# Optimization experiments

Measured on AMD Instinct MI355X. Metric: run time of the kernel, lower is better.

## Reference

```python
import jax, jax.numpy as jnp
import numpy as np

N_NODES = 50000
N_EDGES = 800000
D_FEAT = 64


def setup_inputs() -> dict:
    key = jax.random.key(0)
    k1, k2, k3 = jax.random.split(key, 3)
    xs = jax.random.normal(k1, (N_NODES, D_FEAT), dtype=jnp.float32)
    src = jax.random.randint(k2, (N_EDGES,), 0, N_NODES, dtype=jnp.int32)
    dst = jax.random.randint(k3, (N_EDGES,), 0, N_NODES, dtype=jnp.int32)
    return {"xs": xs, "src": src, "dst": dst}


def reference(xs, src, dst):
    # Edge-list scatter-mean: for each edge (src=ee, dst=i), accumulate
    # xs[ee] into bucket i, then divide by the bucket count.
    gathered = xs[src]                                   # [E, D]
    sums = jax.ops.segment_sum(gathered, dst, num_segments=N_NODES)  # [N, D]
    counts = jax.ops.segment_sum(
        jnp.ones((src.shape[0],), dtype=xs.dtype), dst, num_segments=N_NODES
    )                                                    # [N]
    # Original only emits groups that appear; here empty groups yield 0.
    return sums / jnp.maximum(counts, 1.0)[:, None]
```

## Files before the change

### kernel.cpp

```cpp
#include <hip/hip_runtime.h>

#define N_NODES 50000
#define N_EDGES 800000
#define D_FEAT 64

#define NPART 200
#define EPP (N_EDGES / NPART)
#define BIG_SHIFT 9
#define BIG_NODES 512
#define NBIG ((N_NODES + BIG_NODES - 1) / BIG_NODES)
#define SCAP 12288

__global__ __launch_bounds__(1024) void part_hist_kernel(const int* __restrict__ dst,
                                                         int* __restrict__ histBB) {
    __shared__ int h[NBIG];
    int t = threadIdx.x, blk = blockIdx.x;
    if (t < NBIG) h[t] = 0;
    __syncthreads();
    int base = blk * EPP;
    for (int i = t; i < EPP; i += 1024)
        atomicAdd(&h[dst[base + i] >> BIG_SHIFT], 1);
    __syncthreads();
    if (t < NBIG) histBB[blk * NBIG + t] = h[t];
}

__global__ void col_scan_kernel(const int* __restrict__ histBB,
                                int* __restrict__ baseBB,
                                int* __restrict__ binTot) {
    __shared__ int lds[256];
    int bin = blockIdx.x, t = threadIdx.x;
    int v = (t < NPART) ? histBB[t * NBIG + bin] : 0;
    lds[t] = v;
    __syncthreads();
    for (int off = 1; off < 256; off <<= 1) {
        int x = (t >= off) ? lds[t - off] : 0;
        __syncthreads();
        lds[t] += x;
        __syncthreads();
    }
    if (t < NPART) baseBB[t * NBIG + bin] = lds[t] - v;
    if (t == 255) binTot[bin] = lds[255];
}

__global__ void bin_scan_kernel(const int* __restrict__ binTot, int* __restrict__ binBase) {
    __shared__ int wsum[2];
    int t = threadIdx.x;
    int v = (t < NBIG) ? binTot[t] : 0;
    int lane = t & 63, wave = t >> 6;
    int incl = v;
    #pragma unroll
    for (int o = 1; o < 64; o <<= 1) { int x = __shfl_up(incl, o); if (lane >= o) incl += x; }
    if (lane == 63) wsum[wave] = incl;
    __syncthreads();
    int base = (wave == 1) ? wsum[0] : 0;
    if (t < NBIG) binBase[t] = base + incl - v;
    if (t == NBIG - 1) binBase[NBIG] = base + incl;
}

__global__ __launch_bounds__(1024) void part_scatter_kernel(const int* __restrict__ src,
                                                            const int* __restrict__ dst,
                                                            const int* __restrict__ baseBB,
                                                            const int* __restrict__ binBase,
                                                            unsigned int* __restrict__ staging) {
    __shared__ int cur[NBIG];
    int t = threadIdx.x, blk = blockIdx.x;
    if (t < NBIG) cur[t] = binBase[t] + baseBB[blk * NBIG + t];
    __syncthreads();
    int base = blk * EPP;
    for (int i = t; i < EPP; i += 1024) {
        int d = dst[base + i];
        int bin = d >> BIG_SHIFT;
        int pos = atomicAdd(&cur[bin], 1);
        staging[pos] = (unsigned int)src[base + i] |
                       ((unsigned int)(d & (BIG_NODES - 1)) << 16);
    }
}

__global__ __launch_bounds__(512) void sort512_kernel(const unsigned int* __restrict__ staging,
                                                      const int* __restrict__ binBase,
                                                      unsigned short* __restrict__ esorted,
                                                      int* __restrict__ offs) {
    __shared__ int cnt[BIG_NODES];
    __shared__ int cur[BIG_NODES];
    __shared__ unsigned short list[SCAP];
    __shared__ int wsum[8];
    int bin = blockIdx.x, t = threadIdx.x;
    int lo = binBase[bin], hi = binBase[bin + 1];
    int n = hi - lo;
    int nodeLo = bin << BIG_SHIFT;

    cnt[t] = 0;
    __syncthreads();
    for (int i = lo + t; i < hi; i += 512)
        atomicAdd(&cnt[(staging[i] >> 16) & (BIG_NODES - 1)], 1);
    __syncthreads();

    int v = cnt[t];
    int lane = t & 63, wave = t >> 6;
    int incl = v;
    #pragma unroll
    for (int o = 1; o < 64; o <<= 1) { int x = __shfl_up(incl, o); if (lane >= o) incl += x; }
    if (lane == 63) wsum[wave] = incl;
    __syncthreads();
    int wbase = 0;
    #pragma unroll
    for (int w = 0; w < 8; ++w) wbase += (w < wave) ? wsum[w] : 0;
    int excl = wbase + incl - v;
    cur[t] = excl;

    int node = nodeLo + t;
    if (node < N_NODES) offs[node] = lo + excl;
    if (bin == NBIG - 1 && t == 0) offs[N_NODES] = N_EDGES;
    __syncthreads();

    if (n <= SCAP) {
        for (int i = lo + t; i < hi; i += 512) {
            unsigned int pk = staging[i];
            int p = atomicAdd(&cur[(pk >> 16) & (BIG_NODES - 1)], 1);
            list[p] = (unsigned short)pk;
        }
        __syncthreads();
        for (int i = t; i < n; i += 512)
            esorted[lo + i] = list[i];
    } else {
        for (int i = lo + t; i < hi; i += 512) {
            unsigned int pk = staging[i];
            int p = atomicAdd(&cur[(pk >> 16) & (BIG_NODES - 1)], 1);
            esorted[lo + p] = (unsigned short)pk;
        }
    }
}

__global__ __launch_bounds__(256) void csr_pull_kernel(const float* __restrict__ xs,
                                                       const unsigned short* __restrict__ esorted,
                                                       const int* __restrict__ offs,
                                                       float* __restrict__ out) {
    int tid = blockIdx.x * 256 + threadIdx.x;
    int node = tid >> 4;
    int c = tid & 15;
    int beg = offs[node];
    int end = offs[node + 1];
    int deg = end - beg;
    float4 acc = make_float4(0.f, 0.f, 0.f, 0.f);
    for (int j0 = 0; j0 < deg; j0 += 16) {
        int rem = deg - j0;
        int m = rem < 16 ? rem : 16;
        int myid = (c < m) ? (int)__builtin_nontemporal_load(esorted + beg + j0 + c) : 0;
        if (m == 16) {
            #pragma unroll
            for (int k = 0; k < 16; ++k) {
                int s = __shfl(myid, k, 16);
                const float4 v = *reinterpret_cast<const float4*>(xs + s * D_FEAT + c * 4);
                acc.x += v.x; acc.y += v.y; acc.z += v.z; acc.w += v.w;
            }
        } else {
            for (int k = 0; k < m; ++k) {
                int s = __shfl(myid, k, 16);
                const float4 v = *reinterpret_cast<const float4*>(xs + s * D_FEAT + c * 4);
                acc.x += v.x; acc.y += v.y; acc.z += v.z; acc.w += v.w;
            }
        }
    }
    float inv = 1.0f / fmaxf((float)deg, 1.0f);
    float* op = out + (size_t)node * D_FEAT + c * 4;
    __builtin_nontemporal_store(acc.x * inv, op + 0);
    __builtin_nontemporal_store(acc.y * inv, op + 1);
    __builtin_nontemporal_store(acc.z * inv, op + 2);
    __builtin_nontemporal_store(acc.w * inv, op + 3);
}


__global__ void scatter_kernel(const float* __restrict__ xs,
                               const int* __restrict__ src,
                               const int* __restrict__ dst,
                               float* __restrict__ sums,
                               float* __restrict__ counts) {
    int tid = blockIdx.x * blockDim.x + threadIdx.x;
    int e = tid >> 4;
    int c = tid & 15;
    if (e >= N_EDGES) return;
    int s = src[e];
    int d = dst[e];
    const float4 v = *reinterpret_cast<const float4*>(xs + (size_t)s * D_FEAT + c * 4);
    float* outp = sums + (size_t)d * D_FEAT + c * 4;
    atomicAdd(outp + 0, v.x);
    atomicAdd(outp + 1, v.y);
    atomicAdd(outp + 2, v.z);
    atomicAdd(outp + 3, v.w);
    if (c == 0) atomicAdd(counts + d, 1.0f);
}

__global__ void divide_kernel(float* __restrict__ out, const float* __restrict__ counts) {
    int tid = blockIdx.x * blockDim.x + threadIdx.x;
    if (tid >= N_NODES * D_FEAT / 4) return;
    int node = tid >> 4;
    float inv = 1.0f / fmaxf(counts[node], 1.0f);
    float4 v = reinterpret_cast<const float4*>(out)[tid];
    v.x *= inv; v.y *= inv; v.z *= inv; v.w *= inv;
    reinterpret_cast<float4*>(out)[tid] = v;
}


extern "C" void kernel_launch(void* const* d_in, const int* in_sizes, int n_in,
                              void* d_out, int out_size, void* d_ws, size_t ws_size,
                              hipStream_t stream) {
    const float* xs  = (const float*)d_in[0];
    const int*   src = (const int*)d_in[1];
    const int*   dst = (const int*)d_in[2];
    float* out = (float*)d_out;

    size_t need = (size_t)(2 * NPART * NBIG + NBIG + (NBIG + 1) + (N_NODES + 1)) * sizeof(int)
                + (size_t)N_EDGES * sizeof(unsigned int)
                + (size_t)N_EDGES * sizeof(unsigned short);
    if (ws_size < need) {
        float* counts = (float*)d_ws;
        hipMemsetAsync(out, 0, (size_t)N_NODES * D_FEAT * sizeof(float), stream);
        hipMemsetAsync(counts, 0, (size_t)N_NODES * sizeof(float), stream);
        scatter_kernel<<<(N_EDGES * 16 + 255) / 256, 256, 0, stream>>>(xs, src, dst, out, counts);
        divide_kernel<<<(N_NODES * D_FEAT / 4 + 255) / 256, 256, 0, stream>>>(out, counts);
        return;
    }

    int* ws = (int*)d_ws;
    int* histBB  = ws;
    int* baseBB  = histBB + NPART * NBIG;
    int* binTot  = baseBB + NPART * NBIG;
    int* binBase = binTot + NBIG;
    int* offs    = binBase + NBIG + 1;
    unsigned int* staging = (unsigned int*)(offs + N_NODES + 1);
    unsigned short* esorted = (unsigned short*)(staging + N_EDGES);

    part_hist_kernel<<<NPART, 1024, 0, stream>>>(dst, histBB);
    col_scan_kernel<<<NBIG, 256, 0, stream>>>(histBB, baseBB, binTot);
    bin_scan_kernel<<<1, 128, 0, stream>>>(binTot, binBase);
    part_scatter_kernel<<<NPART, 1024, 0, stream>>>(src, dst, baseBB, binBase, staging);
    sort512_kernel<<<NBIG, 512, 0, stream>>>(staging, binBase, esorted, offs);
    csr_pull_kernel<<<(N_NODES * 16) / 256, 256, 0, stream>>>(xs, esorted, offs, out);
}
```

Before: 124.4 us.

## Fuse CSR build phases into one cooperative kernel with grid syncs

```diff
diff --git a/kernel.cpp b/kernel.cpp
--- a/kernel.cpp
+++ b/kernel.cpp
@@ -1,4 +1,7 @@
 #include <hip/hip_runtime.h>
+#include <hip/hip_cooperative_groups.h>
+
+namespace cg = cooperative_groups;
 
 #define N_NODES 50000
 #define N_EDGES 800000
@@ -9,125 +12,114 @@
 #define BIG_SHIFT 9
 #define BIG_NODES 512
 #define NBIG ((N_NODES + BIG_NODES - 1) / BIG_NODES)
-#define SCAP 12288
-
-__global__ __launch_bounds__(1024) void part_hist_kernel(const int* __restrict__ dst,
-                                                         int* __restrict__ histBB) {
-    __shared__ int h[NBIG];
-    int t = threadIdx.x, blk = blockIdx.x;
-    if (t < NBIG) h[t] = 0;
-    __syncthreads();
-    int base = blk * EPP;
-    for (int i = t; i < EPP; i += 1024)
-        atomicAdd(&h[dst[base + i] >> BIG_SHIFT], 1);
-    __syncthreads();
-    if (t < NBIG) histBB[blk * NBIG + t] = h[t];
-}
-
-__global__ void col_scan_kernel(const int* __restrict__ histBB,
-                                int* __restrict__ baseBB,
-                                int* __restrict__ binTot) {
-    __shared__ int lds[256];
-    int bin = blockIdx.x, t = threadIdx.x;
-    int v = (t < NPART) ? histBB[t * NBIG + bin] : 0;
-    lds[t] = v;
-    __syncthreads();
-    for (int off = 1; off < 256; off <<= 1) {
-        int x = (t >= off) ? lds[t - off] : 0;
-        __syncthreads();
-        lds[t] += x;
-        __syncthreads();
-    }
-    if (t < NPART) baseBB[t * NBIG + bin] = lds[t] - v;
-    if (t == 255) binTot[bin] = lds[255];
-}
-
-__global__ void bin_scan_kernel(const int* __restrict__ binTot, int* __restrict__ binBase) {
-    __shared__ int wsum[2];
+#define GRID_BUILD 200
+
+__global__ __launch_bounds__(256, 4) void build_kernel(
+    const int* __restrict__ src, const int* __restrict__ dst,
+    int* __restrict__ histBB, int* __restrict__ baseBB,
+    int* __restrict__ binTot, int* __restrict__ binBase,
+    int* __restrict__ offs,
+    unsigned int* __restrict__ staging,
+    unsigned short* __restrict__ esorted)
+{
+    cg::grid_group grid = cg::this_grid();
+    __shared__ int sa[512];
+    __shared__ int sb[512];
     int t = threadIdx.x;
-    int v = (t < NBIG) ? binTot[t] : 0;
-    int lane = t & 63, wave = t >> 6;
-    int incl = v;
-    #pragma unroll
-    for (int o = 1; o < 64; o <<= 1) { int x = __shfl_up(incl, o); if (lane >= o) incl += x; }
-    if (lane == 63) wsum[wave] = incl;
-    __syncthreads();
-    int base = (wave == 1) ? wsum[0] : 0;
-    if (t < NBIG) binBase[t] = base + incl - v;
-    if (t == NBIG - 1) binBase[NBIG] = base + incl;
-}
-
-__global__ __launch_bounds__(1024) void part_scatter_kernel(const int* __restrict__ src,
-                                                            const int* __restrict__ dst,
-                                                            const int* __restrict__ baseBB,
-                                                            const int* __restrict__ binBase,
-                                                            unsigned int* __restrict__ staging) {
-    __shared__ int cur[NBIG];
-    int t = threadIdx.x, blk = blockIdx.x;
-    if (t < NBIG) cur[t] = binBase[t] + baseBB[blk * NBIG + t];
-    __syncthreads();
-    int base = blk * EPP;
-    for (int i = t; i < EPP; i += 1024) {
-        int d = dst[base + i];
-        int bin = d >> BIG_SHIFT;
-        int pos = atomicAdd(&cur[bin], 1);
-        staging[pos] = (unsigned int)src[base + i] |
-                       ((unsigned int)(d & (BIG_NODES - 1)) << 16);
-    }
-}
-
-__global__ __launch_bounds__(512) void sort512_kernel(const unsigned int* __restrict__ staging,
-                                                      const int* __restrict__ binBase,
-                                                      unsigned short* __restrict__ esorted,
-                                                      int* __restrict__ offs) {
-    __shared__ int cnt[BIG_NODES];
-    __shared__ int cur[BIG_NODES];
-    __shared__ unsigned short list[SCAP];
-    __shared__ int wsum[8];
-    int bin = blockIdx.x, t = threadIdx.x;
-    int lo = binBase[bin], hi = binBase[bin + 1];
-    int n = hi - lo;
-    int nodeLo = bin << BIG_SHIFT;
-
-    cnt[t] = 0;
-    __syncthreads();
-    for (int i = lo + t; i < hi; i += 512)
-        atomicAdd(&cnt[(staging[i] >> 16) & (BIG_NODES - 1)], 1);
-    __syncthreads();
-
-    int v = cnt[t];
-    int lane = t & 63, wave = t >> 6;
-    int incl = v;
-    #pragma unroll
-    for (int o = 1; o < 64; o <<= 1) { int x = __shfl_up(incl, o); if (lane >= o) incl += x; }
-    if (lane == 63) wsum[wave] = incl;
-    __syncthreads();
-    int wbase = 0;
-    #pragma unroll
-    for (int w = 0; w < 8; ++w) wbase += (w < wave) ? wsum[w] : 0;
-    int excl = wbase + incl - v;
-    cur[t] = excl;
-
-    int node = nodeLo + t;
-    if (node < N_NODES) offs[node] = lo + excl;
-    if (bin == NBIG - 1 && t == 0) offs[N_NODES] = N_EDGES;
-    __syncthreads();
-
-    if (n <= SCAP) {
-        for (int i = lo + t; i < hi; i += 512) {
+
+    for (int p = blockIdx.x; p < NPART; p += gridDim.x) {
+        if (t < NBIG) sa[t] = 0;
+        __syncthreads();
+        int base = p * EPP;
+        for (int i = t; i < EPP; i += 256)
+            atomicAdd(&sa[dst[base + i] >> BIG_SHIFT], 1);
+        __syncthreads();
+        if (t < NBIG) histBB[p * NBIG + t] = sa[t];
+        __syncthreads();
+    }
+    grid.sync();
+
+    for (int bin = blockIdx.x; bin < NBIG; bin += gridDim.x) {
+        int v = (t < NPART) ? histBB[t * NBIG + bin] : 0;
+        sa[t] = v;
+        __syncthreads();
+        for (int off = 1; off < 256; off <<= 1) {
+            int x = (t >= off) ? sa[t - off] : 0;
+            __syncthreads();
+            sa[t] += x;
+            __syncthreads();
+        }
+        if (t < NPART) baseBB[t * NBIG + bin] = sa[t] - v;
+        if (t == 255) binTot[bin] = sa[255];
+        __syncthreads();
+    }
+    grid.sync();
+
+    if (blockIdx.x == 0) {
+        int v = (t < NBIG) ? binTot[t] : 0;
+        int lane = t & 63, wave = t >> 6;
+        int incl = v;
+        #pragma unroll
+        for (int o = 1; o < 64; o <<= 1) { int x = __shfl_up(incl, o); if (lane >= o) incl += x; }
+        if (lane == 63) sb[wave] = incl;
+        __syncthreads();
+        int wbase = 0;
+        #pragma unroll
+        for (int w = 0; w < 4; ++w) wbase += (w < wave) ? sb[w] : 0;
+        if (t < NBIG) binBase[t] = wbase + incl - v;
+        if (t == NBIG - 1) binBase[NBIG] = wbase + incl;
+    }
+    grid.sync();
+
+    for (int p = blockIdx.x; p < NPART; p += gridDim.x) {
+        if (t < NBIG) sa[t] = binBase[t] + baseBB[p * NBIG + t];
+        __syncthreads();
+        int base = p * EPP;
+        for (int i = t; i < EPP; i += 256) {
+            int d = dst[base + i];
+            int bin = d >> BIG_SHIFT;
+            int pos = atomicAdd(&sa[bin], 1);
+            staging[pos] = (unsigned int)src[base + i] |
+                           ((unsigned int)(d & (BIG_NODES - 1)) << 16);
+        }
+        __syncthreads();
+    }
+    grid.sync();
+
+    for (int bin = blockIdx.x; bin < NBIG; bin += gridDim.x) {
+        int lo = binBase[bin], hi = binBase[bin + 1];
+        sa[t] = 0; sa[t + 256] = 0;
+        __syncthreads();
+        for (int i = lo + t; i < hi; i += 256)
+            atomicAdd(&sa[(staging[i] >> 16) & (BIG_NODES - 1)], 1);
+        __syncthreads();
+        int c0 = sa[2 * t], c1 = sa[2 * t + 1];
+        int pv = c0 + c1;
+        int lane = t & 63, wave = t >> 6;
+        int incl = pv;
+        #pragma unroll
+        for (int o = 1; o < 64; o <<= 1) { int x = __shfl_up(incl, o); if (lane >= o) incl += x; }
+        if (lane == 63) sb[wave] = incl;
+        __syncthreads();
+        int wbase = 0;
+        #pragma unroll
+        for (int w = 0; w < 4; ++w) wbase += (w < wave) ? sb[w] : 0;
+        int eh = wbase + incl - pv;
+        __syncthreads();
+        int e0 = eh, e1 = eh + c0;
+        sb[2 * t] = lo + e0;
+        sb[2 * t + 1] = lo + e1;
+        int node = (bin << BIG_SHIFT) + 2 * t;
+        if (node < N_NODES) offs[node] = lo + e0;
+        if (node + 1 < N_NODES) offs[node + 1] = lo + e1;
+        if (bin == NBIG - 1 && t == 0) offs[N_NODES] = N_EDGES;
+        __syncthreads();
+        for (int i = lo + t; i < hi; i += 256) {
             unsigned int pk = staging[i];
-            int p = atomicAdd(&cur[(pk >> 16) & (BIG_NODES - 1)], 1);
-            list[p] = (unsigned short)pk;
+            int p = atomicAdd(&sb[(pk >> 16) & (BIG_NODES - 1)], 1);
+            esorted[p] = (unsigned short)pk;
         }
         __syncthreads();
-        for (int i = t; i < n; i += 512)
-            esorted[lo + i] = list[i];
-    } else {
-        for (int i = lo + t; i < hi; i += 512) {
-            unsigned int pk = staging[i];
-            int p = atomicAdd(&cur[(pk >> 16) & (BIG_NODES - 1)], 1);
-            esorted[lo + p] = (unsigned short)pk;
-        }
     }
 }
 
@@ -170,34 +162,108 @@
 }
 
 
-__global__ void scatter_kernel(const float* __restrict__ xs,
-                               const int* __restrict__ src,
-                               const int* __restrict__ dst,
-                               float* __restrict__ sums,
-                               float* __restrict__ counts) {
-    int tid = blockIdx.x * blockDim.x + threadIdx.x;
-    int e = tid >> 4;
-    int c = tid & 15;
-    if (e >= N_EDGES) return;
-    int s = src[e];
-    int d = dst[e];
-    const float4 v = *reinterpret_cast<const float4*>(xs + (size_t)s * D_FEAT + c * 4);
-    float* outp = sums + (size_t)d * D_FEAT + c * 4;
-    atomicAdd(outp + 0, v.x);
-    atomicAdd(outp + 1, v.y);
-    atomicAdd(outp + 2, v.z);
-    atomicAdd(outp + 3, v.w);
-    if (c == 0) atomicAdd(counts + d, 1.0f);
-}
-
-__global__ void divide_kernel(float* __restrict__ out, const float* __restrict__ counts) {
-    int tid = blockIdx.x * blockDim.x + threadIdx.x;
-    if (tid >= N_NODES * D_FEAT / 4) return;
-    int node = tid >> 4;
-    float inv = 1.0f / fmaxf(counts[node], 1.0f);
-    float4 v = reinterpret_cast<const float4*>(out)[tid];
-    v.x *= inv; v.y *= inv; v.z *= inv; v.w *= inv;
-    reinterpret_cast<float4*>(out)[tid] = v;
+__global__ __launch_bounds__(1024) void part_hist_kernel(const int* __restrict__ dst,
+                                                         int* __restrict__ histBB) {
+    __shared__ int h[NBIG];
+    int t = threadIdx.x, blk = blockIdx.x;
+    if (t < NBIG) h[t] = 0;
+    __syncthreads();
+    int base = blk * EPP;
+    for (int i = t; i < EPP; i += 1024)
+        atomicAdd(&h[dst[base + i] >> BIG_SHIFT], 1);
+    __syncthreads();
+    if (t < NBIG) histBB[blk * NBIG + t] = h[t];
+}
+
+__global__ void col_scan_kernel(const int* __restrict__ histBB,
+                                int* __restrict__ baseBB,
+                                int* __restrict__ binTot) {
+    __shared__ int lds[256];
+    int bin = blockIdx.x, t = threadIdx.x;
+    int v = (t < NPART) ? histBB[t * NBIG + bin] : 0;
+    lds[t] = v;
+    __syncthreads();
+    for (int off = 1; off < 256; off <<= 1) {
+        int x = (t >= off) ? lds[t - off] : 0;
+        __syncthreads();
+        lds[t] += x;
+        __syncthreads();
+    }
+    if (t < NPART) baseBB[t * NBIG + bin] = lds[t] - v;
+    if (t == 255) binTot[bin] = lds[255];
+}
+
+__global__ void bin_scan_kernel(const int* __restrict__ binTot, int* __restrict__ binBase) {
+    __shared__ int wsum[2];
+    int t = threadIdx.x;
+    int v = (t < NBIG) ? binTot[t] : 0;
+    int lane = t & 63, wave = t >> 6;
+    int incl = v;
+    #pragma unroll
+    for (int o = 1; o < 64; o <<= 1) { int x = __shfl_up(incl, o); if (lane >= o) incl += x; }
+    if (lane == 63) wsum[wave] = incl;
+    __syncthreads();
+    int base = (wave == 1) ? wsum[0] : 0;
+    if (t < NBIG) binBase[t] = base + incl - v;
+    if (t == NBIG - 1) binBase[NBIG] = base + incl;
+}
+
+__global__ __launch_bounds__(1024) void part_scatter_kernel(const int* __restrict__ src,
+                                                            const int* __restrict__ dst,
+                                                            const int* __restrict__ baseBB,
+                                                            const int* __restrict__ binBase,
+                                                            unsigned int* __restrict__ staging) {
+    __shared__ int cur[NBIG];
+    int t = threadIdx.x, blk = blockIdx.x;
+    if (t < NBIG) cur[t] = binBase[t] + baseBB[blk * NBIG + t];
+    __syncthreads();
+    int base = blk * EPP;
+    for (int i = t; i < EPP; i += 1024) {
+        int d = dst[base + i];
+        int bin = d >> BIG_SHIFT;
+        int pos = atomicAdd(&cur[bin], 1);
+        staging[pos] = (unsigned int)src[base + i] |
+                       ((unsigned int)(d & (BIG_NODES - 1)) << 16);
+    }
+}
+
+__global__ __launch_bounds__(512) void sort512_kernel(const unsigned int* __restrict__ staging,
+                                                      const int* __restrict__ binBase,
+                                                      unsigned short* __restrict__ esorted,
+                                                      int* __restrict__ offs) {
+    __shared__ int cnt[BIG_NODES];
+    __shared__ int cur[BIG_NODES];
+    __shared__ int wsum[8];
+    int bin = blockIdx.x, t = threadIdx.x;
+    int lo = binBase[bin], hi = binBase[bin + 1];
+    int nodeLo = bin << BIG_SHIFT;
+
+    cnt[t] = 0;
+    __syncthreads();
+    for (int i = lo + t; i < hi; i += 512)
+        atomicAdd(&cnt[(staging[i] >> 16) & (BIG_NODES - 1)], 1);
+    __syncthreads();
+    int v = cnt[t];
+    int lane = t & 63, wave = t >> 6;
+    int incl = v;
+    #pragma unroll
+    for (int o = 1; o < 64; o <<= 1) { int x = __shfl_up(incl, o); if (lane >= o) incl += x; }
+    if (lane == 63) wsum[wave] = incl;
+    __syncthreads();
+    int wbase = 0;
+    #pragma unroll
+    for (int w = 0; w < 8; ++w) wbase += (w < wave) ? wsum[w] : 0;
+    int excl = wbase + incl - v;
+    cur[t] = lo + excl;
+    int node = nodeLo + t;
+    if (node < N_NODES) offs[node] = lo + excl;
+    if (bin == NBIG - 1 && t == 0) offs[N_NODES] = N_EDGES;
+    __syncthreads();
+    for (int i = lo + t; i < hi; i += 512) {
+        unsigned int pk = staging[i];
+        int p = atomicAdd(&cur[(pk >> 16) & (BIG_NODES - 1)], 1);
+        esorted[p] = (unsigned short)pk;
+    }
 }
 
 
@@ -208,18 +274,6 @@
     const int*   src = (const int*)d_in[1];
     const int*   dst = (const int*)d_in[2];
     float* out = (float*)d_out;
-
-    size_t need = (size_t)(2 * NPART * NBIG + NBIG + (NBIG + 1) + (N_NODES + 1)) * sizeof(int)
-                + (size_t)N_EDGES * sizeof(unsigned int)
-                + (size_t)N_EDGES * sizeof(unsigned short);
-    if (ws_size < need) {
-        float* counts = (float*)d_ws;
-        hipMemsetAsync(out, 0, (size_t)N_NODES * D_FEAT * sizeof(float), stream);
-        hipMemsetAsync(counts, 0, (size_t)N_NODES * sizeof(float), stream);
-        scatter_kernel<<<(N_EDGES * 16 + 255) / 256, 256, 0, stream>>>(xs, src, dst, out, counts);
-        divide_kernel<<<(N_NODES * D_FEAT / 4 + 255) / 256, 256, 0, stream>>>(out, counts);
-        return;
-    }
 
     int* ws = (int*)d_ws;
     int* histBB  = ws;
@@ -230,10 +284,22 @@
     unsigned int* staging = (unsigned int*)(offs + N_NODES + 1);
     unsigned short* esorted = (unsigned short*)(staging + N_EDGES);
 
-    part_hist_kernel<<<NPART, 1024, 0, stream>>>(dst, histBB);
-    col_scan_kernel<<<NBIG, 256, 0, stream>>>(histBB, baseBB, binTot);
-    bin_scan_kernel<<<1, 128, 0, stream>>>(binTot, binBase);
-    part_scatter_kernel<<<NPART, 1024, 0, stream>>>(src, dst, baseBB, binBase, staging);
-    sort512_kernel<<<NBIG, 512, 0, stream>>>(staging, binBase, esorted, offs);
+    const int* src_a = src; const int* dst_a = dst;
+    int* histBB_a = histBB; int* baseBB_a = baseBB; int* binTot_a = binTot;
+    int* binBase_a = binBase; int* offs_a = offs;
+    unsigned int* staging_a = staging; unsigned short* esorted_a = esorted;
+    void* args[] = { (void*)&src_a, (void*)&dst_a, (void*)&histBB_a, (void*)&baseBB_a,
+                     (void*)&binTot_a, (void*)&binBase_a, (void*)&offs_a,
+                     (void*)&staging_a, (void*)&esorted_a };
+    hipError_t err = hipLaunchCooperativeKernel((const void*)build_kernel,
+                                                dim3(GRID_BUILD), dim3(256),
+                                                args, 0, stream);
+    if (err != hipSuccess) {
+        part_hist_kernel<<<NPART, 1024, 0, stream>>>(dst, histBB);
+        col_scan_kernel<<<NBIG, 256, 0, stream>>>(histBB, baseBB, binTot);
+        bin_scan_kernel<<<1, 128, 0, stream>>>(binTot, binBase);
+        part_scatter_kernel<<<NPART, 1024, 0, stream>>>(src, dst, baseBB, binBase, staging);
+        sort512_kernel<<<NBIG, 512, 0, stream>>>(staging, binBase, esorted, offs);
+    }
     csr_pull_kernel<<<(N_NODES * 16) / 256, 256, 0, stream>>>(xs, esorted, offs, out);
 }
```

Result: slower. 240.4 us (+93.2%).
